# Kernel optimization log

Hardware: AMD Instinct MI355X
Metric: run time of the kernel (lower is better)

The kernel has to match this reference:

```python
import jax, jax.numpy as jnp
import numpy as np

BM = 192  # query block size (kernel hard-coded to BM=192)


def setup_inputs() -> dict:
    key = jax.random.key(0)
    k1, k2, k3 = jax.random.split(key, 3)
    B, H, S, D = 1, 12, 3840, 128
    q = jax.random.normal(k1, (B, H, S, D), dtype=jnp.float32)
    k = jax.random.normal(k2, (B, H, S, D), dtype=jnp.float32)
    v = jax.random.normal(k3, (B, H, S, D), dtype=jnp.float32)
    topk = 1024
    return {"q": q, "k": k, "v": v, "topk": topk}


def reference(q, k, v, topk):
    # Chipmunk SparseDiffAttn core pipeline:
    # 1) dense_colsum_attn: dense attention whose probs are column-summed per
    #    192-query block to produce block scores bs [B,H,QG,S]
    # 2) topk index selection per query group (mask -> indices)
    # 3) csp_attn: block-sparse attention where each 192-query group attends
    #    only to its selected top-k keys
    B, H, S, D = q.shape
    QG = S // BM
    scale = 1.0 / np.sqrt(D)

    # --- dense colsum attention (scoring pass) ---
    scores = jnp.einsum('bhqd,bhkd->bhqk', q, k) * scale      # [B,H,S,S]
    probs = jax.nn.softmax(scores, axis=-1)                   # [B,H,S,S]
    # column-sum of attention probs within each 192-query block
    bs = probs.reshape(B, H, QG, BM, S).sum(axis=-2)          # [B,H,QG,S]

    # --- topk mask -> per-group key indices ---
    _, inds = jax.lax.top_k(bs, topk)                         # [B,H,QG,TK] int32

    # --- block-sparse gather attention (csp_attn) ---
    # gather selected keys/values per query group
    gather = jax.vmap(jax.vmap(lambda kv, idx: kv[idx]))      # over B, H
    kg = gather(k, inds)                                      # [B,H,QG,TK,D]
    vg = gather(v, inds)                                      # [B,H,QG,TK,D]
    qg = q.reshape(B, H, QG, BM, D)                           # [B,H,QG,BM,D]

    s2 = jnp.einsum('bhgqd,bhgkd->bhgqk', qg, kg) * scale     # [B,H,QG,BM,TK]
    p2 = jax.nn.softmax(s2, axis=-1)
    o = jnp.einsum('bhgqk,bhgkd->bhgqd', p2, vg)              # [B,H,QG,BM,D]
    return o.reshape(B, H, S, D)
```

## Files before the change

kernel.cpp:

```cpp
#include <hip/hip_runtime.h>
#include <math.h>


#define HH 12
#define SS 3840
#define DD 128
#define QGn 20
#define TKn 1024
#define NROWS (HH * QGn)
#define HS (HH * SS)
#define NT 60
#define TCH 3072
#define SCALE_D 0.08838834764831845
#define SCALE_F 0.08838834764831845f

typedef short short8 __attribute__((ext_vector_type(8)));
typedef short short4v __attribute__((ext_vector_type(4)));
typedef float f32x4 __attribute__((ext_vector_type(4)));

#define MFMA(a, b, c) __builtin_amdgcn_mfma_f32_16x16x32_bf16(a, b, c, 0, 0, 0)
#define MFMA_B16(c, a, b) \
  c = __builtin_amdgcn_mfma_f32_16x16x32_bf16(a, b, c, 0, 0, 0)

typedef __attribute__((address_space(3))) unsigned int lds_u32;
typedef const __attribute__((address_space(1))) unsigned int glb_u32;

__device__ __forceinline__ unsigned short bf_rne(float x) {
  unsigned u = __float_as_uint(x);
  u = (u + 0x7fffu + ((u >> 16) & 1u)) >> 16;
  return (unsigned short)u;
}
__device__ __forceinline__ float bf_f(unsigned short b) {
  return __uint_as_float(((unsigned)b) << 16);
}
__device__ __forceinline__ void split3(float f, unsigned short& a,
                                       unsigned short& b, unsigned short& c) {
  a = bf_rne(f);
  float r = f - bf_f(a);
  b = bf_rne(r);
  r = r - bf_f(b);
  c = bf_rne(r);
}
__device__ __forceinline__ void split2(float f, unsigned short& a,
                                       unsigned short& b) {
  a = bf_rne(f);
  float r = f - bf_f(a);
  b = bf_rne(r);
}
__device__ __forceinline__ short8 ldfrag(const unsigned short* base, int chunk) {
  return *(const short8*)&base[(size_t)chunk * 8];
}

__global__ __launch_bounds__(1024) void presplit_kernel(
    const float* __restrict__ q, const float* __restrict__ k,
    unsigned short* __restrict__ qsplit, unsigned short* __restrict__ ksplit) {
  const int t = threadIdx.x;
  const int lane = t & 63;
  const int u = t >> 6;
  const int kc = u & 3, kt = u >> 2;
  const int ln = lane & 15, quad = lane >> 4;
  const int c = blockIdx.x;
  const int h = blockIdx.y;
  const float* src = blockIdx.z ? k : q;
  unsigned short* dst = blockIdx.z ? ksplit : qsplit;

  const float* p =
      &src[(size_t)(h * SS + c * 64 + kt * 16 + ln) * DD + kc * 32 + quad * 8];
  float b8[8];
  *(float4*)&b8[0] = *(const float4*)&p[0];
  *(float4*)&b8[4] = *(const float4*)&p[4];
  __attribute__((aligned(16))) unsigned short f0[8], f1[8], f2[8];
#pragma unroll
  for (int e = 0; e < 8; ++e) split3(b8[e], f0[e], f1[e], f2[e]);
  size_t base =
      ((size_t)(h * NT + c) * TCH + ((kt * 4 + kc) * 3) * 64 + lane) * 8;
  *(uint4*)&dst[base + 0] = *(const uint4*)f0;
  *(uint4*)&dst[base + 512] = *(const uint4*)f1;
  *(uint4*)&dst[base + 1024] = *(const uint4*)f2;
}

__global__ __launch_bounds__(256) void stats_mfma(
    const unsigned short* __restrict__ qsplit,
    const unsigned short* __restrict__ ksplit,
    double* __restrict__ lpart) {
  __shared__ __align__(16) unsigned short Bs[3][6144];
  const int t = threadIdx.x;
  const int w = t >> 6;
  const int lane = t & 63;
  const int ln = lane & 15;
  const int quad = lane >> 4;
  const int h = blockIdx.y;
  const int nq = blockIdx.z;
  const int q0 = blockIdx.x * 128 + w * 32;
  const int tq = blockIdx.x * 2 + (w >> 1);
  const int ktA = (w & 1) * 2;

  short8 A[2][4][3];
  {
    const unsigned short* qb = &qsplit[(size_t)(h * NT + tq) * TCH * 8];
#pragma unroll
    for (int s = 0; s < 2; ++s)
#pragma unroll
      for (int kc = 0; kc < 4; ++kc)
#pragma unroll
        for (int cm = 0; cm < 3; ++cm)
          A[s][kc][cm] =
              ldfrag(qb, (((ktA + s) * 4 + kc) * 3 + cm) * 64 + lane);
  }

  double racc[2][4];
#pragma unroll
  for (int s = 0; s < 2; ++s)
#pragma unroll
    for (int r = 0; r < 4; ++r) racc[s][r] = 0.0;

  const unsigned short* kq = &ksplit[(size_t)(h * NT + nq * 15) * TCH * 8];

#define STG_S(slot, j)                                                     \
  do {                                                                     \
    const unsigned short* src_ = kq + (size_t)(j) * 6144 + t * 8;          \
    __builtin_amdgcn_global_load_lds((glb_u32*)(src_),                     \
        (lds_u32*)&Bs[slot][w * 512], 16, 0, 0);                           \
    __builtin_amdgcn_global_load_lds((glb_u32*)(src_ + 2048),              \
        (lds_u32*)&Bs[slot][2048 + w * 512], 16, 0, 0);                    \
    __builtin_amdgcn_global_load_lds((glb_u32*)(src_ + 4096),              \
        (lds_u32*)&Bs[slot][4096 + w * 512], 16, 0, 0);                    \
  } while (0)

  const f32x4 z = {0.f, 0.f, 0.f, 0.f};
  f32x4 C[2][3];

  STG_S(0, 0);

  int cur = 0;
#pragma unroll 1
  for (int j = 0; j < 60; ++j) {
    __builtin_amdgcn_sched_barrier(0);
    if (j < 59) {
      const int nxt = (cur == 2) ? 0 : cur + 1;
      STG_S(nxt, j + 1);
      asm volatile("s_waitcnt vmcnt(3)" ::: "memory");
    } else {
      asm volatile("s_waitcnt vmcnt(0)" ::: "memory");
    }
    __builtin_amdgcn_s_barrier();
    __builtin_amdgcn_sched_barrier(0);
    __builtin_amdgcn_s_setprio(1);
    if (j > 0) {
#pragma unroll
      for (int s = 0; s < 2; ++s)
#pragma unroll
        for (int r = 0; r < 4; ++r) {
          float sv = (C[s][0][r] + C[s][1][r]) + C[s][2][r];
          racc[s][r] += (double)__expf(sv * SCALE_F);
        }
    }
    const unsigned short* Bp = &Bs[cur][0];
#pragma unroll
    for (int kc = 0; kc < 4; ++kc) {
      short8 B0 = *(const short8*)&Bp[(kc * 3 + 0) * 512 + lane * 8];
      short8 B1 = *(const short8*)&Bp[(kc * 3 + 1) * 512 + lane * 8];
      short8 B2 = *(const short8*)&Bp[(kc * 3 + 2) * 512 + lane * 8];
#pragma unroll
      for (int s = 0; s < 2; ++s) {
        if (kc == 0) {
          C[s][0] = MFMA(A[s][0][0], B0, z);
          C[s][1] = MFMA(A[s][0][0], B1, z);
          C[s][1] = MFMA(A[s][0][1], B0, C[s][1]);
          C[s][0] = MFMA(A[s][0][1], B1, C[s][0]);
          C[s][2] = MFMA(A[s][0][2], B0, z);
          C[s][2] = MFMA(A[s][0][0], B2, C[s][2]);
        } else {
          MFMA_B16(C[s][0], A[s][kc][0], B0);
          MFMA_B16(C[s][1], A[s][kc][0], B1);
          MFMA_B16(C[s][1], A[s][kc][1], B0);
          MFMA_B16(C[s][0], A[s][kc][1], B1);
          MFMA_B16(C[s][2], A[s][kc][2], B0);
          MFMA_B16(C[s][2], A[s][kc][0], B2);
        }
      }
    }
    __builtin_amdgcn_s_setprio(0);
    cur = (cur == 2) ? 0 : cur + 1;
  }
#undef STG_S

#pragma unroll
  for (int s = 0; s < 2; ++s)
#pragma unroll
    for (int r = 0; r < 4; ++r) {
      float sv = (C[s][0][r] + C[s][1][r]) + C[s][2][r];
      racc[s][r] += (double)__expf(sv * SCALE_F);
    }

#pragma unroll
  for (int s = 0; s < 2; ++s)
#pragma unroll
    for (int r = 0; r < 4; ++r) {
      double v = racc[s][r];
      v += __shfl_xor(v, 1);
      v += __shfl_xor(v, 2);
      v += __shfl_xor(v, 4);
      v += __shfl_xor(v, 8);
      if (ln == 0)
        lpart[(size_t)nq * HS + h * SS + q0 + s * 16 + quad * 4 + r] = v;
    }
}

__global__ __launch_bounds__(256) void colsum_mfma(
    const unsigned short* __restrict__ qsplit,
    const unsigned short* __restrict__ ksplit,
    const double* __restrict__ lpart, double* __restrict__ bs) {
  __shared__ double rls[192];
  __shared__ __align__(16) unsigned short As[3][6144];
  const int t = threadIdx.x;
  const int w = t >> 6;
  const int lane = t & 63;
  const int ln = lane & 15;
  const int quad = lane >> 4;
  const int h = blockIdx.z, g = blockIdx.y;
  const int k0 = blockIdx.x * 128 + w * 32;
  const int tk = blockIdx.x * 2 + (w >> 1);
  const int ktB = (w & 1) * 2;

  short8 Bk[2][4][3];
  {
    const unsigned short* kb = &ksplit[(size_t)(h * NT + tk) * TCH * 8];
#pragma unroll
    for (int s = 0; s < 2; ++s)
#pragma unroll
      for (int kc = 0; kc < 4; ++kc)
#pragma unroll
        for (int cm = 0; cm < 3; ++cm)
          Bk[s][kc][cm] =
              ldfrag(kb, (((ktB + s) * 4 + kc) * 3 + cm) * 64 + lane);
  }

  if (t < 192) {
    size_t qi = h * SS + g * 192 + t;
    rls[t] = 1.0 / (lpart[qi] + lpart[HS + qi] + lpart[2 * (size_t)HS + qi] +
                    lpart[3 * (size_t)HS + qi]);
  }
  __syncthreads();

  double cacc[2] = {0.0, 0.0};

  const unsigned short* qg = &qsplit[(size_t)(h * NT + g * 3) * TCH * 8];

#define STG_C(slot, j)                                                     \
  do {                                                                     \
    const unsigned short* src_ = qg + (size_t)(j) * 6144 + t * 8;          \
    __builtin_amdgcn_global_load_lds((glb_u32*)(src_),                     \
        (lds_u32*)&As[slot][w * 512], 16, 0, 0);                           \
    __builtin_amdgcn_global_load_lds((glb_u32*)(src_ + 2048),              \
        (lds_u32*)&As[slot][2048 + w * 512], 16, 0, 0);                    \
    __builtin_amdgcn_global_load_lds((glb_u32*)(src_ + 4096),              \
        (lds_u32*)&As[slot][4096 + w * 512], 16, 0, 0);                    \
  } while (0)

  const f32x4 z = {0.f, 0.f, 0.f, 0.f};
  f32x4 C[2][3];

  STG_C(0, 0);

  int cur = 0;
#pragma unroll 1
  for (int j = 0; j < 12; ++j) {
    __builtin_amdgcn_sched_barrier(0);
    if (j < 11) {
      const int nxt = (cur == 2) ? 0 : cur + 1;
      STG_C(nxt, j + 1);
      asm volatile("s_waitcnt vmcnt(3)" ::: "memory");
    } else {
      asm volatile("s_waitcnt vmcnt(0)" ::: "memory");
    }
    __builtin_amdgcn_s_barrier();
    __builtin_amdgcn_sched_barrier(0);
    __builtin_amdgcn_s_setprio(1);
    if (j > 0) {
      const int qprev = (j - 1) * 16;
#pragma unroll
      for (int s = 0; s < 2; ++s)
#pragma unroll
        for (int r = 0; r < 4; ++r) {
          float p = __expf(((C[s][0][r] + C[s][1][r]) + C[s][2][r]) * SCALE_F);
          cacc[s] += (double)p * rls[qprev + quad * 4 + r];
        }
    }
    const unsigned short* Ap = &As[cur][0];
#pragma unroll
    for (int kc = 0; kc < 4; ++kc) {
      short8 A0 = *(const short8*)&Ap[(kc * 3 + 0) * 512 + lane * 8];
      short8 A1 = *(const short8*)&Ap[(kc * 3 + 1) * 512 + lane * 8];
      short8 A2 = *(const short8*)&Ap[(kc * 3 + 2) * 512 + lane * 8];
#pragma unroll
      for (int s = 0; s < 2; ++s) {
        if (kc == 0) {
          C[s][0] = MFMA(A0, Bk[s][0][0], z);
          C[s][1] = MFMA(A1, Bk[s][0][0], z);
          C[s][1] = MFMA(A0, Bk[s][0][1], C[s][1]);
          C[s][0] = MFMA(A1, Bk[s][0][1], C[s][0]);
          C[s][2] = MFMA(A2, Bk[s][0][0], z);
          C[s][2] = MFMA(A0, Bk[s][0][2], C[s][2]);
        } else {
          MFMA_B16(C[s][0], A0, Bk[s][kc][0]);
          MFMA_B16(C[s][1], A1, Bk[s][kc][0]);
          MFMA_B16(C[s][1], A0, Bk[s][kc][1]);
          MFMA_B16(C[s][0], A1, Bk[s][kc][1]);
          MFMA_B16(C[s][2], A2, Bk[s][kc][0]);
          MFMA_B16(C[s][2], A0, Bk[s][kc][2]);
        }
      }
    }
    __builtin_amdgcn_s_setprio(0);
    cur = (cur == 2) ? 0 : cur + 1;
  }
#undef STG_C

#pragma unroll
  for (int s = 0; s < 2; ++s)
#pragma unroll
    for (int r = 0; r < 4; ++r) {
      float p = __expf(((C[s][0][r] + C[s][1][r]) + C[s][2][r]) * SCALE_F);
      cacc[s] += (double)p * rls[176 + quad * 4 + r];
    }

#pragma unroll
  for (int s = 0; s < 2; ++s) {
    double v = cacc[s];
    v += __shfl_xor(v, 16);
    v += __shfl_xor(v, 32);
    if (quad == 0)
      bs[(size_t)(h * QGn + g) * SS + k0 + s * 16 + ln] = v;
  }
}

__global__ __launch_bounds__(256) void topk3_kernel(
    const double* __restrict__ bs, int* __restrict__ inds,
    double* __restrict__ bnd_val, int* __restrict__ bnd_idx) {
  __shared__ unsigned long long u[SS];
  __shared__ int hist[256];
  __shared__ int sfx[256];
  __shared__ int s_bin, s_r;
  __shared__ int c_gt, c_eq;
  __shared__ unsigned long long rv[256];
  __shared__ int ri[256];
  const int t = threadIdx.x;
  const int row = blockIdx.x;
  const double* vals = bs + (size_t)row * SS;

  for (int i = t; i < SS; i += 256)
    u[i] = (unsigned long long)__double_as_longlong(vals[i]);

  unsigned long long pref = 0ull;
  int r = TKn;
  for (int shift = 56; shift >= 0; shift -= 8) {
    hist[t] = 0;
    __syncthreads();
    unsigned long long himask =
        (shift == 56) ? 0ull : (0xFFFFFFFFFFFFFFFFull << (shift + 8));
    for (int i = t; i < SS; i += 256) {
      unsigned long long uv = u[i];
      if ((uv & himask) == (pref & himask))
        atomicAdd(&hist[(int)((uv >> shift) & 255)], 1);
    }
    __syncthreads();
    sfx[t] = hist[t];
    __syncthreads();
#pragma unroll
    for (int off = 1; off < 256; off <<= 1) {
      int v = (t + off < 256) ? sfx[t + off] : 0;
      __syncthreads();
      sfx[t] += v;
      __syncthreads();
    }
    {
      int St = sfx[t];
      int Sn = (t == 255) ? 0 : sfx[t + 1];
      if (St >= r && Sn < r) {
        s_bin = t;
        s_r = r - Sn;
      }
    }
    if (t == 0) {
      c_gt = 0;
      c_eq = 0;
    }
    __syncthreads();
    pref |= ((unsigned long long)s_bin) << shift;
    r = s_r;
    __syncthreads();
  }
  const int G = TKn - r;
  int* out = inds + (size_t)row * TKn;
  unsigned long long mb = 0ull;
  int mbi = -1;
  for (int i = t; i < SS; i += 256) {
    unsigned long long uv = u[i];
    if (uv > pref) {
      int p = atomicAdd(&c_gt, 1);
      out[p] = i;
    } else if (uv == pref) {
      int e = atomicAdd(&c_eq, 1);
      if (e < r) out[G + e] = i;
      if (e == r - 1) bnd_idx[row * 2 + 0] = i;
    } else if (uv > mb) {
      mb = uv;
      mbi = i;
    }
  }
  rv[t] = mb;
  ri[t] = mbi;
  __syncthreads();
  for (int s2 = 128; s2 > 0; s2 >>= 1) {
    if (t < s2 && rv[t + s2] > rv[t]) {
      rv[t] = rv[t + s2];
      ri[t] = ri[t + s2];
    }
    __syncthreads();
  }
  if (t == 0) {
    bnd_val[row * 2 + 0] = __longlong_as_double((long long)pref);
    bnd_val[row * 2 + 1] = __longlong_as_double((long long)rv[0]);
    bnd_idx[row * 2 + 1] = ri[0];
  }
}

__global__ __launch_bounds__(256) void exact_rl_kernel(
    const float* __restrict__ q, const float* __restrict__ k,
    const double* __restrict__ bnd_val, double* __restrict__ rl_exact) {
  __shared__ double gmin[256];
  __shared__ int grow[256];
  __shared__ double qd[DD];
  __shared__ double red[256];
  const int t = threadIdx.x;
  {
    double gv = 1e300;
    int rr = -1;
    if (t < NROWS) {
      gv = bnd_val[t * 2 + 0] - bnd_val[t * 2 + 1];
      rr = t;
    }
    gmin[t] = gv;
    grow[t] = rr;
    __syncthreads();
    for (int s2 = 128; s2 > 0; s2 >>= 1) {
      if (t < s2 && gmin[t + s2] < gmin[t]) {
        gmin[t] = gmin[t + s2];
        grow[t] = grow[t + s2];
      }
      __syncthreads();
    }
  }
  const int row = grow[0];
  const int h = row / QGn, g = row % QGn;
  const float* qp = &q[(size_t)(h * SS + g * 192 + blockIdx.x) * DD];
  if (t < DD) qd[t] = (double)qp[t];
  __syncthreads();
  double l = 0.0;
  for (int kk = t; kk < SS; kk += 256) {
    const float* kp = &k[(size_t)(h * SS + kk) * DD];
    double s = 0.0;
#pragma unroll 4
    for (int d = 0; d < DD; d += 4) {
      float4 kv = *(const float4*)&kp[d];
      s += qd[d] * (double)kv.x + qd[d + 1] * (double)kv.y +
           qd[d + 2] * (double)kv.z + qd[d + 3] * (double)kv.w;
    }
    l += exp(s * SCALE_D);
  }
  red[t] = l;
  __syncthreads();
  for (int s2 = 128; s2 > 0; s2 >>= 1) {
    if (t < s2) red[t] += red[t + s2];
    __syncthreads();
  }
  if (t == 0) rl_exact[blockIdx.x] = 1.0 / red[0];
}

__global__ __launch_bounds__(256) void exact_pair_kernel(
    const float* __restrict__ q, const float* __restrict__ k,
    const double* __restrict__ bnd_val, const int* __restrict__ bnd_idx,
    const double* __restrict__ rl_exact, int* __restrict__ inds) {
  __shared__ double gmin[256];
  __shared__ int grow[256];
  __shared__ double redX[256], redY[256];
  const int t = threadIdx.x;
  {
    double gv = 1e300;
    int rr = -1;
    if (t < NROWS) {
      gv = bnd_val[t * 2 + 0] - bnd_val[t * 2 + 1];
      rr = t;
    }
    gmin[t] = gv;
    grow[t] = rr;
    __syncthreads();
    for (int s2 = 128; s2 > 0; s2 >>= 1) {
      if (t < s2 && gmin[t + s2] < gmin[t]) {
        gmin[t] = gmin[t + s2];
        grow[t] = grow[t + s2];
      }
      __syncthreads();
    }
  }
  const int row = grow[0];
  const int kept = bnd_idx[row * 2 + 0], drop = bnd_idx[row * 2 + 1];
  const int h = row / QGn, g = row % QGn;
  double px = 0.0, py = 0.0;
  if (t < 192) {
    const float* qp = &q[(size_t)(h * SS + g * 192 + t) * DD];
    const float* kx = &k[(size_t)(h * SS + kept) * DD];
    const float* ky = &k[(size_t)(h * SS + drop) * DD];
    double sx = 0.0, sy = 0.0;
#pragma unroll 4
    for (int d = 0; d < DD; ++d) {
      double qv = (double)qp[d];
      sx += qv * (double)kx[d];
      sy += qv * (double)ky[d];
    }
    double rv = rl_exact[t];
    px = exp(sx * SCALE_D) * rv;
    py = exp(sy * SCALE_D) * rv;
  }
  redX[t] = px;
  redY[t] = py;
  __syncthreads();
  for (int s2 = 128; s2 > 0; s2 >>= 1) {
    if (t < s2) { redX[t] += redX[t + s2]; redY[t] += redY[t + s2]; }
    __syncthreads();
  }
  if (t == 0)
    inds[(size_t)row * TKn + (TKn - 1)] = (redX[0] <= redY[0]) ? kept : drop;
}

__global__ __launch_bounds__(768, 3) void sparse_attn_mfma(
    const float* __restrict__ q, const float* __restrict__ v,
    const int* __restrict__ inds, const unsigned short* __restrict__ ksplit,
    float* __restrict__ out) {
  __shared__ __align__(16) unsigned short ksmN[16 * 512];
  __shared__ __align__(16) unsigned short vsm[2][128][40];
  __shared__ __align__(16) unsigned short pbuf[12][2][16][36];
  __shared__ float rls_sm[12][16];
  const int t = threadIdx.x;
  const int w = t >> 6;
  const int lane = t & 63;
  const int ln = lane & 15;
  const int quad = lane >> 4;
  const int g = blockIdx.x, h = blockIdx.y;
  const int* ip = &inds[(size_t)(h * QGn + g) * TKn];
  const unsigned short* kbh = &ksplit[(size_t)(h * NT) * (TCH * 8)];
  const int qs0 = (w % 6) * 2;
  const int dtb = (w / 6) * 4;

  short8 A[4][2];
  {
    const float* qp =
        &q[(size_t)(h * SS + g * 192 + w * 16 + ln) * DD + quad * 8];
#pragma unroll
    for (int kc = 0; kc < 4; ++kc) {
      float b8[8];
      *(float4*)&b8[0] = *(const float4*)&qp[kc * 32];
      *(float4*)&b8[4] = *(const float4*)&qp[kc * 32 + 4];
      short8 f0, f1;
#pragma unroll
      for (int e = 0; e < 8; ++e) {
        unsigned short x0, x1;
        split2(b8[e], x0, x1);
        f0[e] = (short)x0; f1[e] = (short)x1;
      }
      A[kc][0] = f0; A[kc][1] = f1;
    }
  }

  f32x4 Oa[4], Ob[4];
#pragma unroll
  for (int d2 = 0; d2 < 4; ++d2) {
    Oa[d2] = (f32x4){0.f, 0.f, 0.f, 0.f};
    Ob[d2] = (f32x4){0.f, 0.f, 0.f, 0.f};
  }
  float lacc[4] = {0.f, 0.f, 0.f, 0.f};

  const int kk = t >> 3;
  const int sub = t & 7;
  const int sW = w >> 1;
  const int c0 = w * 4;

  int gkA = 0;
  float4 rv4[4];
  if (w < 4) {
    gkA = ip[sW * 16 + ln];
    int gkV = ip[kk];
    const float* vp = &v[(size_t)(h * SS + gkV) * DD + sub * 16];
#pragma unroll
    for (int e4 = 0; e4 < 4; ++e4) rv4[e4] = *(const float4*)&vp[e4 * 4];
  }

  for (int kt = 0; kt < TKn; kt += 32) {
    __builtin_amdgcn_s_barrier();
    __builtin_amdgcn_sched_barrier(0);
    if (w < 4) {
      const bool more = (kt + 32 < TKn);
      int gkVn = 0, gkAn = 0;
      if (more) {
        gkVn = ip[kt + 32 + kk];
        gkAn = ip[kt + 32 + sW * 16 + ln];
      }
      {
        const unsigned short* rowp = kbh + (size_t)(gkA >> 6) * (TCH * 8) +
                                     ((gkA & 15) + 16 * quad) * 8;
        const int ktile = (gkA >> 4) & 3;
#pragma unroll
        for (int i = 0; i < 4; ++i) {
          const int c16 = c0 + i;
          const int kc = (c16 >> 1) & 3;
          const int cm = c16 & 1;
          __builtin_amdgcn_global_load_lds(
              (glb_u32*)(rowp + ((ktile * 4 + kc) * 3 + cm) * 512),
              (lds_u32*)&ksmN[c16 * 512], 16, 0, 0);
        }
      }
#pragma unroll
      for (int e4 = 0; e4 < 4; ++e4) {
        float4 vv = rv4[e4];
        ushort4 v0, v1;
        split2(vv.x, v0.x, v1.x);
        split2(vv.y, v0.y, v1.y);
        split2(vv.z, v0.z, v1.z);
        split2(vv.w, v0.w, v1.w);
        int d0 = sub * 16 + e4 * 4;
        vsm[0][d0 + 0][kk] = v0.x; vsm[1][d0 + 0][kk] = v1.x;
        vsm[0][d0 + 1][kk] = v0.y; vsm[1][d0 + 1][kk] = v1.y;
        vsm[0][d0 + 2][kk] = v0.z; vsm[1][d0 + 2][kk] = v1.z;
        vsm[0][d0 + 3][kk] = v0.w; vsm[1][d0 + 3][kk] = v1.w;
      }
      if (more) {
        const float* vp = &v[(size_t)(h * SS + gkVn) * DD + sub * 16];
#pragma unroll
        for (int e4 = 0; e4 < 4; ++e4) rv4[e4] = *(const float4*)&vp[e4 * 4];
        asm volatile("s_waitcnt vmcnt(4) lgkmcnt(0)" ::: "memory");
        gkA = gkAn;
      } else {
        asm volatile("s_waitcnt vmcnt(0) lgkmcnt(0)" ::: "memory");
      }
    }
    __builtin_amdgcn_s_barrier();
    __builtin_amdgcn_sched_barrier(0);

#pragma unroll
    for (int s = 0; s < 2; ++s) {
      f32x4 C0 = {0.f, 0.f, 0.f, 0.f};
      f32x4 C1 = C0;
      __builtin_amdgcn_s_setprio(1);
#pragma unroll
      for (int kc = 0; kc < 4; ++kc) {
        short8 B0 = *(const short8*)&ksmN[(s * 8 + kc * 2 + 0) * 512 + lane * 8];
        short8 B1 = *(const short8*)&ksmN[(s * 8 + kc * 2 + 1) * 512 + lane * 8];
        MFMA_B16(C0, A[kc][0], B0);
        MFMA_B16(C1, A[kc][1], B0);
        MFMA_B16(C1, A[kc][0], B1);
      }
      __builtin_amdgcn_s_setprio(0);
#pragma unroll
      for (int r = 0; r < 4; ++r) {
        float pv = __expf((C0[r] + C1[r]) * SCALE_F);
        lacc[r] += pv;
        unsigned short p0, p1;
        split2(pv, p0, p1);
        pbuf[w][0][quad * 4 + r][s * 16 + ln] = p0;
        pbuf[w][1][quad * 4 + r][s * 16 + ln] = p1;
      }
    }
    asm volatile("s_waitcnt lgkmcnt(0)" ::: "memory");
    __builtin_amdgcn_s_barrier();
    __builtin_amdgcn_sched_barrier(0);

    short8 P0a, P1a, P0b, P1b;
    {
      const unsigned short* pb;
      short4v lo, hi;
      pb = &pbuf[qs0][0][ln][quad * 8];
      lo = *(const short4v*)pb; hi = *(const short4v*)(pb + 4);
      P0a = __builtin_shufflevector(lo, hi, 0, 1, 2, 3, 4, 5, 6, 7);
      pb = &pbuf[qs0][1][ln][quad * 8];
      lo = *(const short4v*)pb; hi = *(const short4v*)(pb + 4);
      P1a = __builtin_shufflevector(lo, hi, 0, 1, 2, 3, 4, 5, 6, 7);
      pb = &pbuf[qs0 + 1][0][ln][quad * 8];
      lo = *(const short4v*)pb; hi = *(const short4v*)(pb + 4);
      P0b = __builtin_shufflevector(lo, hi, 0, 1, 2, 3, 4, 5, 6, 7);
      pb = &pbuf[qs0 + 1][1][ln][quad * 8];
      lo = *(const short4v*)pb; hi = *(const short4v*)(pb + 4);
      P1b = __builtin_shufflevector(lo, hi, 0, 1, 2, 3, 4, 5, 6, 7);
    }
    __builtin_amdgcn_s_setprio(1);
#pragma unroll
    for (int d2 = 0; d2 < 4; ++d2) {
      const int dt = dtb + d2;
      short8 V0 = *(const short8*)&vsm[0][dt * 16 + ln][quad * 8];
      short8 V1 = *(const short8*)&vsm[1][dt * 16 + ln][quad * 8];
      MFMA_B16(Oa[d2], P0a, V0);
      MFMA_B16(Oa[d2], P1a, V0);
      MFMA_B16(Oa[d2], P0a, V1);
      MFMA_B16(Ob[d2], P0b, V0);
      MFMA_B16(Ob[d2], P1b, V0);
      MFMA_B16(Ob[d2], P0b, V1);
    }
    __builtin_amdgcn_s_setprio(0);
  }

#pragma unroll
  for (int r = 0; r < 4; ++r) {
    float l = lacc[r];
    l += __shfl_xor(l, 1);
    l += __shfl_xor(l, 2);
    l += __shfl_xor(l, 4);
    l += __shfl_xor(l, 8);
    float rl = 1.f / l;
    if (ln == 0) rls_sm[w][quad * 4 + r] = rl;
  }
  __syncthreads();

#pragma unroll
  for (int half = 0; half < 2; ++half) {
    const int qs = qs0 + half;
#pragma unroll
    for (int r = 0; r < 4; ++r) {
      float rlv = rls_sm[qs][quad * 4 + r];
      float* op =
          &out[(size_t)(h * SS + g * 192 + qs * 16 + quad * 4 + r) * DD];
#pragma unroll
      for (int d2 = 0; d2 < 4; ++d2) {
        float ov = half ? Ob[d2][r] : Oa[d2][r];
        op[(dtb + d2) * 16 + ln] = ov * rlv;
      }
    }
  }
}

extern "C" void kernel_launch(void* const* d_in, const int* in_sizes, int n_in,
                              void* d_out, int out_size, void* d_ws, size_t ws_size,
                              hipStream_t stream) {
  const float* q = (const float*)d_in[0];
  const float* k = (const float*)d_in[1];
  const float* v = (const float*)d_in[2];
  float* out = (float*)d_out;

  const size_t SPLIT_ELEMS = (size_t)HH * NT * TCH * 8;
  unsigned short* qsplit = (unsigned short*)d_ws;
  unsigned short* ksplit = qsplit + SPLIT_ELEMS;
  double* lpart = (double*)(ksplit + SPLIT_ELEMS);
  double* bs = lpart + 4 * (size_t)HS;
  int* inds = (int*)(bs + (size_t)HH * QGn * SS);
  double* bnd_val = (double*)(inds + (size_t)NROWS * TKn);
  int* bnd_idx = (int*)(bnd_val + (size_t)NROWS * 2);
  int* rsel = bnd_idx + NROWS * 2;
  double* rl_exact = (double*)(rsel + 4);

  presplit_kernel<<<dim3(NT, HH, 2), 1024, 0, stream>>>(q, k, qsplit, ksplit);
  stats_mfma<<<dim3(SS / 128, HH, 4), 256, 0, stream>>>(qsplit, ksplit, lpart);
  colsum_mfma<<<dim3(SS / 128, QGn, HH), 256, 0, stream>>>(qsplit, ksplit, lpart, bs);
  topk3_kernel<<<dim3(NROWS), 256, 0, stream>>>(bs, inds, bnd_val, bnd_idx);
  exact_rl_kernel<<<dim3(192), 256, 0, stream>>>(q, k, bnd_val, rl_exact);
  exact_pair_kernel<<<dim3(1), 256, 0, stream>>>(q, k, bnd_val, bnd_idx, rl_exact, inds);
  sparse_attn_mfma<<<dim3(QGn, HH), 768, 0, stream>>>(q, v, inds, ksplit, out);
}
```

Baseline: 734.7 us.

## Have each wave compute PV for its own query rows, dropping cross-wave barrier

The PV stage is reassigned so each wave multiplies its own 16-row P tile against all 8 head-dim tiles, instead of two waves' P tiles against 4 dim tiles. This removes the block-wide barrier between writing P to shared memory and reading it back, and also the shared reciprocal-sum exchange and its final __syncthreads. In exchange each wave reads twice as many V fragments from shared memory per step and holds 8 accumulators. Output normalization now uses the wave's own row sums directly.

```diff
diff --git a/kernel.cpp b/kernel.cpp
--- a/kernel.cpp
+++ b/kernel.cpp
@@ -541,7 +541,6 @@
   __shared__ __align__(16) unsigned short ksmN[16 * 512];
   __shared__ __align__(16) unsigned short vsm[2][128][40];
   __shared__ __align__(16) unsigned short pbuf[12][2][16][36];
-  __shared__ float rls_sm[12][16];
   const int t = threadIdx.x;
   const int w = t >> 6;
   const int lane = t & 63;
@@ -550,8 +549,6 @@
   const int g = blockIdx.x, h = blockIdx.y;
   const int* ip = &inds[(size_t)(h * QGn + g) * TKn];
   const unsigned short* kbh = &ksplit[(size_t)(h * NT) * (TCH * 8)];
-  const int qs0 = (w % 6) * 2;
-  const int dtb = (w / 6) * 4;
 
   short8 A[4][2];
   {
@@ -573,12 +570,9 @@
     }
   }
 
-  f32x4 Oa[4], Ob[4];
-#pragma unroll
-  for (int d2 = 0; d2 < 4; ++d2) {
-    Oa[d2] = (f32x4){0.f, 0.f, 0.f, 0.f};
-    Ob[d2] = (f32x4){0.f, 0.f, 0.f, 0.f};
-  }
+  f32x4 O[8];
+#pragma unroll
+  for (int dt = 0; dt < 8; ++dt) O[dt] = (f32x4){0.f, 0.f, 0.f, 0.f};
   float lacc[4] = {0.f, 0.f, 0.f, 0.f};
 
   const int kk = t >> 3;
@@ -671,39 +665,25 @@
         pbuf[w][1][quad * 4 + r][s * 16 + ln] = p1;
       }
     }
-    asm volatile("s_waitcnt lgkmcnt(0)" ::: "memory");
-    __builtin_amdgcn_s_barrier();
-    __builtin_amdgcn_sched_barrier(0);
-
-    short8 P0a, P1a, P0b, P1b;
+    short8 P0, P1;
     {
-      const unsigned short* pb;
-      short4v lo, hi;
-      pb = &pbuf[qs0][0][ln][quad * 8];
-      lo = *(const short4v*)pb; hi = *(const short4v*)(pb + 4);
-      P0a = __builtin_shufflevector(lo, hi, 0, 1, 2, 3, 4, 5, 6, 7);
-      pb = &pbuf[qs0][1][ln][quad * 8];
-      lo = *(const short4v*)pb; hi = *(const short4v*)(pb + 4);
-      P1a = __builtin_shufflevector(lo, hi, 0, 1, 2, 3, 4, 5, 6, 7);
-      pb = &pbuf[qs0 + 1][0][ln][quad * 8];
-      lo = *(const short4v*)pb; hi = *(const short4v*)(pb + 4);
-      P0b = __builtin_shufflevector(lo, hi, 0, 1, 2, 3, 4, 5, 6, 7);
-      pb = &pbuf[qs0 + 1][1][ln][quad * 8];
-      lo = *(const short4v*)pb; hi = *(const short4v*)(pb + 4);
-      P1b = __builtin_shufflevector(lo, hi, 0, 1, 2, 3, 4, 5, 6, 7);
+      const unsigned short* pb0 = &pbuf[w][0][ln][quad * 8];
+      const unsigned short* pb1 = &pbuf[w][1][ln][quad * 8];
+      short4v lo0 = *(const short4v*)pb0;
+      short4v hi0 = *(const short4v*)(pb0 + 4);
+      short4v lo1 = *(const short4v*)pb1;
+      short4v hi1 = *(const short4v*)(pb1 + 4);
+      P0 = __builtin_shufflevector(lo0, hi0, 0, 1, 2, 3, 4, 5, 6, 7);
+      P1 = __builtin_shufflevector(lo1, hi1, 0, 1, 2, 3, 4, 5, 6, 7);
     }
     __builtin_amdgcn_s_setprio(1);
 #pragma unroll
-    for (int d2 = 0; d2 < 4; ++d2) {
-      const int dt = dtb + d2;
+    for (int dt = 0; dt < 8; ++dt) {
       short8 V0 = *(const short8*)&vsm[0][dt * 16 + ln][quad * 8];
       short8 V1 = *(const short8*)&vsm[1][dt * 16 + ln][quad * 8];
-      MFMA_B16(Oa[d2], P0a, V0);
-      MFMA_B16(Oa[d2], P1a, V0);
-      MFMA_B16(Oa[d2], P0a, V1);
-      MFMA_B16(Ob[d2], P0b, V0);
-      MFMA_B16(Ob[d2], P1b, V0);
-      MFMA_B16(Ob[d2], P0b, V1);
+      MFMA_B16(O[dt], P0, V0);
+      MFMA_B16(O[dt], P1, V0);
+      MFMA_B16(O[dt], P0, V1);
     }
     __builtin_amdgcn_s_setprio(0);
   }
@@ -716,24 +696,10 @@
     l += __shfl_xor(l, 4);
     l += __shfl_xor(l, 8);
     float rl = 1.f / l;
-    if (ln == 0) rls_sm[w][quad * 4 + r] = rl;
-  }
-  __syncthreads();
-
-#pragma unroll
-  for (int half = 0; half < 2; ++half) {
-    const int qs = qs0 + half;
-#pragma unroll
-    for (int r = 0; r < 4; ++r) {
-      float rlv = rls_sm[qs][quad * 4 + r];
-      float* op =
-          &out[(size_t)(h * SS + g * 192 + qs * 16 + quad * 4 + r) * DD];
-#pragma unroll
-      for (int d2 = 0; d2 < 4; ++d2) {
-        float ov = half ? Ob[d2][r] : Oa[d2][r];
-        op[(dtb + d2) * 16 + ln] = ov * rlv;
-      }
-    }
+    float* op =
+        &out[(size_t)(h * SS + g * 192 + w * 16 + quad * 4 + r) * DD];
+#pragma unroll
+    for (int dt = 0; dt < 8; ++dt) op[dt * 16 + ln] = O[dt][r] * rl;
   }
 }
 
```

After: 702.8 us. 1.05x faster.
